# Kernel optimization log

Measured on AMD Instinct MI355X. Metric: run time of the kernel, lower is better.

## Reference

```python
import jax, jax.numpy as jnp
import numpy as np

N = 30000; E = 480000; B = 32
IN_H = 129; IN_P = 15; HID = 64; HEADS = 8; OUT = 129


def gat_conv(x, src, dst, edge_attr, W, a_src, a_dst, We, a_e, bias, concat):
    # PyG GATConv with edge_dim, add_self_loops=True (fill_value='mean'), negative_slope=0.2
    n = x.shape[0]
    H, C = a_src.shape
    ones = jnp.ones((src.shape[0],), x.dtype)
    deg = jax.ops.segment_sum(ones, dst, num_segments=n)
    ea_mean = jax.ops.segment_sum(edge_attr, dst, num_segments=n) / jnp.clip(deg, 1.0)[:, None]
    loop = jnp.arange(n, dtype=src.dtype)
    s = jnp.concatenate([src, loop])
    t = jnp.concatenate([dst, loop])
    ea = jnp.concatenate([edge_attr, ea_mean], axis=0)
    xw = (x @ W).reshape(n, H, C)              # [N,H,C]
    a_s = jnp.sum(xw * a_src, axis=-1)         # [N,H]
    a_d = jnp.sum(xw * a_dst, axis=-1)         # [N,H]
    ew = (ea @ We).reshape(-1, H, C)           # [E2,H,C]
    a_ed = jnp.sum(ew * a_e, axis=-1)          # [E2,H]
    alpha = jax.nn.leaky_relu(a_s[s] + a_d[t] + a_ed, 0.2)
    amax = jax.ops.segment_max(alpha, t, num_segments=n)   # every node has a self-loop
    expa = jnp.exp(alpha - amax[t])
    denom = jax.ops.segment_sum(expa, t, num_segments=n)
    alpha = expa / denom[t]                    # segment softmax over dst
    out = jax.ops.segment_sum(xw[s] * alpha[..., None], t, num_segments=n)  # [N,H,C]
    out = out.reshape(n, H * C) if concat else jnp.mean(out, axis=1)
    return out + bias


def setup_inputs():
    key = jax.random.key(0)
    ks = jax.random.split(key, 40)
    g = lambda k, s: (jax.random.normal(k, s, jnp.float32) * (1.0 / np.sqrt(s[0])))
    d = {}
    d['x_hrtf'] = jax.random.normal(ks[0], (N, IN_H), jnp.float32)
    d['x_pos'] = jax.random.normal(ks[1], (N, IN_P), jnp.float32)
    d['edge_attr_hrtf'] = jax.random.normal(ks[2], (E, 1), jnp.float32)
    d['edge_attr_pos'] = jax.random.normal(ks[3], (E, 1), jnp.float32)
    # hrtf branch, layer 1 (heads=8, concat)
    d['W1h'] = g(ks[4], (IN_H, HEADS * HID)); d['as1h'] = g(ks[5], (HEADS, HID)); d['ad1h'] = g(ks[6], (HEADS, HID))
    d['We1h'] = g(ks[7], (1, HEADS * HID)); d['ae1h'] = g(ks[8], (HEADS, HID)); d['b1h'] = jnp.zeros((HEADS * HID,), jnp.float32)
    # hrtf branch, layer 2 (heads=1, mean)
    d['W2h'] = g(ks[9], (HEADS * HID, OUT)); d['as2h'] = g(ks[10], (1, OUT)); d['ad2h'] = g(ks[11], (1, OUT))
    d['We2h'] = g(ks[12], (1, OUT)); d['ae2h'] = g(ks[13], (1, OUT)); d['b2h'] = jnp.zeros((OUT,), jnp.float32)
    # pos branch, layer 1
    d['W1p'] = g(ks[14], (IN_P, HEADS * HID)); d['as1p'] = g(ks[15], (HEADS, HID)); d['ad1p'] = g(ks[16], (HEADS, HID))
    d['We1p'] = g(ks[17], (1, HEADS * HID)); d['ae1p'] = g(ks[18], (HEADS, HID)); d['b1p'] = jnp.zeros((HEADS * HID,), jnp.float32)
    # pos branch, layer 2
    d['W2p'] = g(ks[19], (HEADS * HID, OUT)); d['as2p'] = g(ks[20], (1, OUT)); d['ad2p'] = g(ks[21], (1, OUT))
    d['We2p'] = g(ks[22], (1, OUT)); d['ae2p'] = g(ks[23], (1, OUT)); d['b2p'] = jnp.zeros((OUT,), jnp.float32)
    # final fc
    d['Wfc'] = g(ks[24], (2 * OUT, 129)); d['bfc'] = jnp.zeros((129,), jnp.float32)
    d['edge_index_hrtf'] = jax.random.randint(ks[25], (2, E), 0, N, jnp.int32)
    d['edge_index_pos'] = jax.random.randint(ks[26], (2, E), 0, N, jnp.int32)
    d['batch'] = ((jnp.arange(N) * B) // N).astype(jnp.int32)  # sorted, equal-sized graphs
    d['num_graphs'] = B
    return d


def reference(x_hrtf, x_pos, edge_attr_hrtf, edge_attr_pos, W1h, as1h, ad1h, We1h, ae1h, b1h, W2h, as2h, ad2h, We2h, ae2h, b2h, W1p, as1p, ad1p, We1p, ae1p, b1p, W2p, as2p, ad2p, We2p, ae2p, b2p, Wfc, bfc, edge_index_hrtf, edge_index_pos, batch, num_graphs):
    sh, th = edge_index_hrtf[0], edge_index_hrtf[1]
    sp, tp = edge_index_pos[0], edge_index_pos[1]
    h = jax.nn.elu(gat_conv(x_hrtf, sh, th, edge_attr_hrtf, W1h, as1h, ad1h, We1h, ae1h, b1h, True))
    h = gat_conv(h, sh, th, edge_attr_hrtf, W2h, as2h, ad2h, We2h, ae2h, b2h, False)
    p = jax.nn.elu(gat_conv(x_pos, sp, tp, edge_attr_pos, W1p, as1p, ad1p, We1p, ae1p, b1p, True))
    p = gat_conv(p, sp, tp, edge_attr_pos, W2p, as2p, ad2p, We2p, ae2p, b2p, False)
    counts = jax.ops.segment_sum(jnp.ones_like(batch), batch, num_segments=num_graphs)
    last = jnp.cumsum(counts) - 1              # last node index of each graph
    z = jnp.concatenate([h[last], p[last]], axis=-1)
    z = z @ Wfc + bfc
    return z[:, None, :]                       # [B,1,129]
```

## Files before the change

### kernel.cpp

```cpp
#include <hip/hip_runtime.h>

#define N_NODES 30000
#define N_EDGES 480000
#define NB      32
#define HEADS   8
#define F1      512
#define OUT_C   129
#define OUT_S   132
#define W1TS    132

#define CAP1   1024
#define MAXD   64
#define NZREG  (8 + 2 * CAP1 + 2 * NB)

#define SHIFT1 12.0f
#define SHIFT2 20.0f

__device__ __forceinline__ float lrelu(float a) { return a > 0.f ? a : 0.2f * a; }

__device__ __forceinline__ int graph_of(int v) { return (int)(((unsigned)v * 2u) / 1875u); }
__device__ __forceinline__ int last_of(int b) { return (int)((((unsigned)(b + 1) * 1875u) + 1u) / 2u) - 1; }
__device__ __forceinline__ bool is_last_node(int v) { return v == last_of(graph_of(v)); }

__global__ void k_prep(const float* We1h, const float* ae1h,
                       const float* We1p, const float* ae1p,
                       const float* We2h, const float* ae2h,
                       const float* We2p, const float* ae2p,
                       const float* __restrict__ W1h, const float* __restrict__ W1p,
                       const float* as1h, const float* as1p,
                       const float* ad1h, const float* ad1p,
                       float* k12, float* __restrict__ w_as, float* __restrict__ w_ad,
                       int* __restrict__ zreg, int* __restrict__ inv1) {
    int gid = blockIdx.x * 256 + threadIdx.x;
    if (gid < 15000) ((int4*)inv1)[gid] = make_int4(-1, -1, -1, -1);
    if (gid < NZREG) zreg[gid] = 0;
    if (blockIdx.x == 0) {
        int t = threadIdx.x;
        if (t < 8) {
            float s = 0.f;
            for (int c = 0; c < 64; c++) s += We1h[t * 64 + c] * ae1h[t * 64 + c];
            k12[t] = s;
        } else if (t < 16) {
            int h = t - 8;
            float s = 0.f;
            for (int c = 0; c < 64; c++) s += We1p[h * 64 + c] * ae1p[h * 64 + c];
            k12[8 + h] = s;
        } else if (t == 16) {
            float s = 0.f;
            for (int c = 0; c < OUT_C; c++) s += We2h[c] * ae2h[c];
            k12[16] = s;
        } else if (t == 17) {
            float s = 0.f;
            for (int c = 0; c < OUT_C; c++) s += We2p[c] * ae2p[c];
            k12[17] = s;
        }
    }
    if (blockIdx.x >= 64 && blockIdx.x < 96) {
        int bb = blockIdx.x - 64;
        int br = bb >> 4, type = (bb >> 3) & 1, h = bb & 7;
        const float* W1 = br ? W1p : W1h;
        const float* a  = type ? (br ? ad1p : ad1h) : (br ? as1p : as1h);
        float* outp = (type ? w_ad : w_as) + (size_t)(br * 8 + h) * W1TS;
        int K = br ? 15 : 129;
        int d = threadIdx.x;
        if (d < K) {
            float s = 0.f;
            for (int c = 0; c < 64; c++) s += W1[(size_t)d * F1 + h * 64 + c] * a[h * 64 + c];
            outp[d] = s;
        }
    }
}

__global__ __launch_bounds__(256) void k_scan2(const int* __restrict__ ei_h,
        const int* __restrict__ ei_p, const float* __restrict__ ea_h,
        const float* __restrict__ ea_p, int* inv1,
        int* degcnt2, int* eb2v, float* eb2e) {
    int br = blockIdx.y;
    const int* ei = br ? ei_p : ei_h;
    const float* ea = br ? ea_p : ea_h;
    const int* src = ei; const int* dst = ei + N_EDGES;
    inv1 += br * N_NODES;
    degcnt2 += br * NB; eb2v += br * NB * MAXD; eb2e += br * NB * MAXD;
    int tid = threadIdx.x;
    if (blockIdx.x == 0 && tid < NB) inv1[last_of(tid)] = -2;
    int base = (blockIdx.x * 256 + tid) * 4;
    if (base >= N_EDGES) return;
    int4 d = *(const int4*)(dst + base);
    int dv[4] = {d.x, d.y, d.z, d.w};
#pragma unroll
    for (int q = 0; q < 4; q++) {
        if (is_last_node(dv[q])) {
            int e = base + q;
            int b = graph_of(dv[q]);
            int slot = atomicAdd(degcnt2 + b, 1);
            if (slot < MAXD) { eb2v[b * MAXD + slot] = src[e]; eb2e[b * MAXD + slot] = ea[e]; }
            inv1[src[e]] = -2;
        }
    }
}

__global__ __launch_bounds__(256) void k_compact1(int* inv1, int* nodes1, int* cnt) {
    __shared__ int s_v[256];
    __shared__ int s_n, s_base;
    int br = blockIdx.y;
    inv1 += br * N_NODES; nodes1 += br * CAP1;
    int* cntp = cnt + br * 4 + 0;
    int tid = threadIdx.x;
    if (tid == 0) s_n = 0;
    __syncthreads();
    int base = (blockIdx.x * 256 + tid) * 4;
    if (base < N_NODES) {
        int4 w = *(const int4*)(inv1 + base);
        int vv[4] = {w.x, w.y, w.z, w.w};
#pragma unroll
        for (int q = 0; q < 4; q++) {
            if (vv[q] == -2) {
                int p = atomicAdd(&s_n, 1);
                if (p < 256) s_v[p] = base + q;
            }
        }
    }
    __syncthreads();
    int n = s_n; if (n > 256) n = 256;
    if (tid == 0) s_base = atomicAdd(cntp, n);
    __syncthreads();
    for (int q = tid; q < n; q += 256) {
        int j = s_base + q;
        if (j < CAP1) { inv1[s_v[q]] = j; nodes1[j] = s_v[q]; }
    }
}

__global__ __launch_bounds__(256) void k_scan1(const int* __restrict__ ei_h,
        const int* __restrict__ ei_p, const float* __restrict__ ea_h,
        const float* __restrict__ ea_p, const int* __restrict__ inv1,
        int* degcnt1, int* ebv1, float* ebe1) {
    int br = blockIdx.y;
    const int* ei = br ? ei_p : ei_h;
    const float* ea = br ? ea_p : ea_h;
    const int* src = ei; const int* dst = ei + N_EDGES;
    inv1 += br * N_NODES;
    degcnt1 += br * CAP1; ebv1 += (size_t)br * CAP1 * MAXD; ebe1 += (size_t)br * CAP1 * MAXD;
    int tid = threadIdx.x;
    int base = (blockIdx.x * 256 + tid) * 4;
    if (base >= N_EDGES) return;
    int4 d = *(const int4*)(dst + base);
    int dv[4] = {d.x, d.y, d.z, d.w};
#pragma unroll
    for (int q = 0; q < 4; q++) {
        int jj = inv1[dv[q]];
        if (jj >= 0) {
            int e = base + q;
            int slot = atomicAdd(degcnt1 + jj, 1);
            if (slot < MAXD) { ebv1[jj * MAXD + slot] = src[e]; ebe1[jj * MAXD + slot] = ea[e]; }
        }
    }
}

__global__ __launch_bounds__(256) void k_agg1x(const int* __restrict__ ebv1,
        const float* __restrict__ ebe1, const int* __restrict__ degcnt1,
        const int* __restrict__ nodes1, const int* cnt,
        const float* __restrict__ x_h, const float* __restrict__ x_p,
        const float* __restrict__ w_as, const float* __restrict__ w_ad,
        const float* __restrict__ k12, const float* __restrict__ b1h,
        const float* __restrict__ b1p, const float* __restrict__ W1h,
        const float* __restrict__ W1p, const float* __restrict__ W2h,
        const float* __restrict__ W2p, const float* __restrict__ as2h,
        const float* __restrict__ as2p, const float* __restrict__ ad2h,
        const float* __restrict__ ad2p,
        float* __restrict__ xw2, float* __restrict__ as2v, float* __restrict__ ad2all) {
    __shared__ float s_x[MAXD + 9][W1TS];
    __shared__ int   s_v[MAXD + 1];
    __shared__ float s_e[MAXD + 1];
    __shared__ float s_ex[(MAXD + 1) * 8];
    __shared__ float s_den[8];
    __shared__ float s_adh[8];
    __shared__ float s_k1[8];
    __shared__ float s_h1[F1];
    __shared__ float s_row[OUT_S];
    int br = blockIdx.y;
    const float* x    = br ? x_p : x_h;
    const float* b1   = br ? b1p : b1h;
    const float* W1   = br ? W1p : W1h;
    const float* W2   = br ? W2p : W2h;
    const float* as2w = br ? as2p : as2h;
    const float* ad2w = br ? ad2p : ad2h;
    const float* wasb = w_as + (size_t)br * 8 * W1TS;
    const float* wadb = w_ad + (size_t)br * 8 * W1TS;
    int K = br ? 15 : 129;
    int n1 = cnt[br * 4 + 0]; if (n1 > CAP1) n1 = CAP1;
    int j = blockIdx.x;
    if (j >= n1) return;
    int tid = threadIdx.x;
    int deg = degcnt1[br * CAP1 + j]; if (deg > MAXD) deg = MAXD;
    const int*   ebv = ebv1 + ((size_t)br * CAP1 + j) * MAXD;
    const float* ebe = ebe1 + ((size_t)br * CAP1 + j) * MAXD;
    if (tid < deg) { s_v[tid] = ebv[tid]; s_e[tid] = ebe[tid]; }
    if (tid == 0) s_v[deg] = nodes1[br * CAP1 + j];
    if (tid >= 72 && tid < 80) s_k1[tid - 72] = k12[br * 8 + (tid - 72)];
    __syncthreads();
    int total = deg + 1;
    for (int k = tid >> 6; k < total; k += 4) {
        const float* xr = x + (size_t)s_v[k] * K;
        for (int d = (tid & 63); d < K; d += 64) s_x[k][d] = xr[d];
    }
    __syncthreads();
    if (tid < 64) {
        float part = (tid < deg) ? s_e[tid] : 0.f;
#pragma unroll
        for (int o = 32; o > 0; o >>= 1) part += __shfl_down(part, o);
        if (tid == 0) s_e[deg] = part / fmaxf((float)deg, 1.f);
    }
    for (int t = tid; t < total * 8 + 8; t += 256) {
        int k, h; const float* wv;
        if (t < total * 8) { k = t >> 3; h = t & 7; wv = wasb + (size_t)h * W1TS; }
        else               { k = deg; h = t - total * 8; wv = wadb + (size_t)h * W1TS; }
        float dot = 0.f;
        for (int d = 0; d < K; d++) dot += s_x[k][d] * wv[d];
        if (t < total * 8) s_ex[t] = dot; else s_adh[h] = dot;
    }
    __syncthreads();
    for (int t = tid; t < total * 8; t += 256) {
        int k = t >> 3, h = t & 7;
        float a = lrelu(s_ex[t] + s_adh[h] + s_e[k] * s_k1[h]);
        s_ex[t] = __expf(a - SHIFT1);
    }
    __syncthreads();
    if (tid >= 192 && tid < 200) {
        int h = tid - 192;
        float d = 0.f;
        for (int k = 0; k < total; k++) d += s_ex[k * 8 + h];
        s_den[h] = d;
    }
    if (tid < K) {
        float acc[8];
#pragma unroll
        for (int h = 0; h < 8; h++) acc[h] = 0.f;
        for (int k = 0; k < total; k++) {
            float xv = s_x[k][tid];
#pragma unroll
            for (int h = 0; h < 8; h++) acc[h] += s_ex[k * 8 + h] * xv;
        }
#pragma unroll
        for (int h = 0; h < 8; h++) s_x[MAXD + 1 + h][tid] = acc[h];
    }
    __syncthreads();
    {
        int h0 = tid >> 6, h1i = h0 + 4;
        float a0 = 0.f, a1 = 0.f;
        for (int d = 0; d < K; d++) {
            float xa0 = s_x[MAXD + 1 + h0][d];
            float xa1 = s_x[MAXD + 1 + h1i][d];
            a0 += xa0 * W1[(size_t)d * F1 + tid];
            a1 += xa1 * W1[(size_t)d * F1 + tid + 256];
        }
        float v0 = a0 / s_den[h0] + b1[tid];
        float v1 = a1 / s_den[h1i] + b1[tid + 256];
        s_h1[tid]       = v0 > 0.f ? v0 : (__expf(v0) - 1.f);
        s_h1[tid + 256] = v1 > 0.f ? v1 : (__expf(v1) - 1.f);
    }
    __syncthreads();
    if (tid < OUT_C) {
        float a = 0.f;
        for (int k = 0; k < F1; k++) a += s_h1[k] * W2[(size_t)k * OUT_C + tid];
        s_row[tid] = a;
        xw2[((size_t)br * CAP1 + j) * OUT_S + tid] = a;
    }
    __syncthreads();
    if (tid < 128) {
        int w = tid >> 6, l = tid & 63;
        const float* av = w ? ad2w : as2w;
        float p = s_row[l] * av[l] + s_row[64 + l] * av[64 + l];
        if (l == 0) p += s_row[128] * av[128];
#pragma unroll
        for (int o = 32; o > 0; o >>= 1) p += __shfl_down(p, o);
        if (l == 0) {
            if (w) ad2all[br * CAP1 + j] = p;
            else   as2v[br * CAP1 + j] = p;
        }
    }
}

__global__ __launch_bounds__(256) void k_agg2fc(const int* __restrict__ eb2v,
        const float* __restrict__ eb2e, const int* __restrict__ degcnt2,
        const int* __restrict__ inv1, const int* cnt,
        const float* __restrict__ as2v, const float* __restrict__ ad2all,
        const float* __restrict__ k12, const float* __restrict__ b2h,
        const float* __restrict__ b2p, const float* __restrict__ xw2,
        const float* __restrict__ Wfc, const float* __restrict__ bfc,
        float* __restrict__ out) {
    __shared__ int   s_j[MAXD + 1];
    __shared__ float s_e[MAXD + 1];
    __shared__ float s_ex[MAXD + 1];
    __shared__ float s_den;
    __shared__ float hcat[2 * OUT_C];
    int b = blockIdx.x;
    int tid = threadIdx.x;
    for (int br = 0; br < 2; br++) {
        const float* b2 = br ? b2p : b2h;
        const int* inv1b = inv1 + br * N_NODES;
        const float* as2vb = as2v + br * CAP1;
        const float* ad2b = ad2all + br * CAP1;
        const float* xw2b = xw2 + (size_t)br * CAP1 * OUT_S;
        float k2 = k12[16 + br];
        int deg = degcnt2[br * NB + b]; if (deg > MAXD) deg = MAXD;
        if (tid < deg) {
            s_j[tid] = inv1b[eb2v[(br * NB + b) * MAXD + tid]];
            s_e[tid] = eb2e[(br * NB + b) * MAXD + tid];
        }
        if (tid == 0) s_j[deg] = inv1b[last_of(b)];
        __syncthreads();
        if (tid < 64) {
            float part = (tid < deg) ? s_e[tid] : 0.f;
#pragma unroll
            for (int o = 32; o > 0; o >>= 1) part += __shfl_down(part, o);
            if (tid == 0) s_e[deg] = part / fmaxf((float)deg, 1.f);
        }
        __syncthreads();
        int total = deg + 1;
        float adv = ad2b[s_j[deg]];
        for (int k = tid; k < total; k += 256)
            s_ex[k] = __expf(lrelu(as2vb[s_j[k]] + adv + s_e[k] * k2) - SHIFT2);
        __syncthreads();
        if (tid == 0) {
            float d = 0.f;
            for (int k = 0; k < total; k++) d += s_ex[k];
            s_den = d;
        }
        __syncthreads();
        if (tid < OUT_C) {
            float acc = 0.f;
            for (int k = 0; k < total; k++)
                acc += s_ex[k] * xw2b[(size_t)s_j[k] * OUT_S + tid];
            hcat[br * OUT_C + tid] = acc / s_den + b2[tid];
        }
        __syncthreads();
    }
    if (tid < OUT_C) {
        float s = bfc[tid];
        for (int k = 0; k < 2 * OUT_C; k++) s += hcat[k] * Wfc[k * OUT_C + tid];
        out[b * OUT_C + tid] = s;
    }
}

extern "C" void kernel_launch(void* const* d_in, const int* in_sizes, int n_in,
                              void* d_out, int out_size, void* d_ws, size_t ws_size,
                              hipStream_t stream) {
    const float* x_h  = (const float*)d_in[0];
    const float* x_p  = (const float*)d_in[1];
    const float* ea_h = (const float*)d_in[2];
    const float* ea_p = (const float*)d_in[3];
    const float* W1h  = (const float*)d_in[4];
    const float* as1h = (const float*)d_in[5];
    const float* ad1h = (const float*)d_in[6];
    const float* We1h = (const float*)d_in[7];
    const float* ae1h = (const float*)d_in[8];
    const float* b1h  = (const float*)d_in[9];
    const float* W2h  = (const float*)d_in[10];
    const float* as2h = (const float*)d_in[11];
    const float* ad2h = (const float*)d_in[12];
    const float* We2h = (const float*)d_in[13];
    const float* ae2h = (const float*)d_in[14];
    const float* b2h  = (const float*)d_in[15];
    const float* W1p  = (const float*)d_in[16];
    const float* as1p = (const float*)d_in[17];
    const float* ad1p = (const float*)d_in[18];
    const float* We1p = (const float*)d_in[19];
    const float* ae1p = (const float*)d_in[20];
    const float* b1p  = (const float*)d_in[21];
    const float* W2p  = (const float*)d_in[22];
    const float* as2p = (const float*)d_in[23];
    const float* ad2p = (const float*)d_in[24];
    const float* We2p = (const float*)d_in[25];
    const float* ae2p = (const float*)d_in[26];
    const float* b2p  = (const float*)d_in[27];
    const float* Wfc  = (const float*)d_in[28];
    const float* bfc  = (const float*)d_in[29];
    const int*   ei_h = (const int*)d_in[30];
    const int*   ei_p = (const int*)d_in[31];

    char* wsb = (char*)d_ws;
    size_t off = 0;
    auto alloc = [&](size_t elems) -> char* {
        char* p = wsb + off;
        off += ((elems * 4 + 255) / 256) * 256;
        return p;
    };
    float*    k12     = (float*)alloc(18);
    int*      zreg    = (int*)alloc(NZREG);
    int*      cnt     = zreg;
    int*      degcnt1 = zreg + 8;
    int*      degcnt2 = zreg + 8 + 2 * CAP1;
    int*      inv1    = (int*)alloc(2 * N_NODES);
    int*      nodes1  = (int*)alloc(2 * CAP1);
    int*      ebv1    = (int*)alloc(2 * (size_t)CAP1 * MAXD);
    float*    ebe1    = (float*)alloc(2 * (size_t)CAP1 * MAXD);
    int*      eb2v    = (int*)alloc(2 * NB * MAXD);
    float*    eb2e    = (float*)alloc(2 * NB * MAXD);
    float*    w_as    = (float*)alloc(2 * 8 * W1TS);
    float*    w_ad    = (float*)alloc(2 * 8 * W1TS);
    float*    xw2     = (float*)alloc(2 * (size_t)CAP1 * OUT_S);
    float*    as2v    = (float*)alloc(2 * CAP1);
    float*    ad2all  = (float*)alloc(2 * CAP1);
    if (off > ws_size) return;

    const int EBLK4 = (N_EDGES / 4 + 255) / 256;
    const int NBLK4 = (N_NODES / 4 + 255) / 256;

    k_prep<<<96, 256, 0, stream>>>(
        We1h, ae1h, We1p, ae1p, We2h, ae2h, We2p, ae2p,
        W1h, W1p, as1h, as1p, ad1h, ad1p,
        k12, w_as, w_ad, zreg, inv1);
    k_scan2<<<dim3(EBLK4, 2), 256, 0, stream>>>(ei_h, ei_p, ea_h, ea_p, inv1,
                                                degcnt2, eb2v, eb2e);
    k_compact1<<<dim3(NBLK4, 2), 256, 0, stream>>>(inv1, nodes1, cnt);
    k_scan1<<<dim3(EBLK4, 2), 256, 0, stream>>>(ei_h, ei_p, ea_h, ea_p, inv1,
                                                degcnt1, ebv1, ebe1);
    k_agg1x<<<dim3(CAP1, 2), 256, 0, stream>>>(ebv1, ebe1, degcnt1, nodes1, cnt,
                                               x_h, x_p, w_as, w_ad, k12, b1h, b1p,
                                               W1h, W1p, W2h, W2p, as2h, as2p, ad2h, ad2p,
                                               xw2, as2v, ad2all);
    k_agg2fc<<<NB, 256, 0, stream>>>(eb2v, eb2e, degcnt2, inv1, cnt,
                                     as2v, ad2all, k12, b2h, b2p, xw2, Wfc, bfc, (float*)d_out);
}
```

Before: 90.51 us.

## Split fused per-node aggregation into batched GEMM kernels with weight reuse

The monolithic per-node kernel that aggregated neighbours and then multiplied each node's features by W1 and W2 is split into three kernels: aggregation only, a tiled layer-1 GEMM over 32-node tiles per head, and a layer-2 GEMM processing two nodes per block against a transposed W2 prepared in the prep kernel. The goal is to reuse weight loads across many nodes instead of re-reading W1/W2 from global memory per node. In exchange it adds two kernel launches and writes and reads intermediate buffers (normalized aggregates, h1) through global memory.

```diff
diff --git a/kernel.cpp b/kernel.cpp
--- a/kernel.cpp
+++ b/kernel.cpp
@@ -12,6 +12,7 @@
 #define CAP1   1024
 #define MAXD   64
 #define NZREG  (8 + 2 * CAP1 + 2 * NB)
+#define TJ     32
 
 #define SHIFT1 12.0f
 #define SHIFT2 20.0f
@@ -27,13 +28,20 @@
                        const float* We2h, const float* ae2h,
                        const float* We2p, const float* ae2p,
                        const float* __restrict__ W1h, const float* __restrict__ W1p,
+                       const float* __restrict__ W2h, const float* __restrict__ W2p,
                        const float* as1h, const float* as1p,
                        const float* ad1h, const float* ad1p,
                        float* k12, float* __restrict__ w_as, float* __restrict__ w_ad,
-                       int* __restrict__ zreg, int* __restrict__ inv1) {
+                       float* __restrict__ W2t2, int* __restrict__ zreg,
+                       int* __restrict__ inv1) {
     int gid = blockIdx.x * 256 + threadIdx.x;
     if (gid < 15000) ((int4*)inv1)[gid] = make_int4(-1, -1, -1, -1);
     if (gid < NZREG) zreg[gid] = 0;
+    if (gid < 512 * OUT_C) {
+        int k = gid / OUT_C, c = gid % OUT_C;
+        W2t2[c * 512 + k] = W2h[gid];
+        W2t2[512 * OUT_C + c * 512 + k] = W2p[gid];
+    }
     if (blockIdx.x == 0) {
         int t = threadIdx.x;
         if (t < 8) {
@@ -55,8 +63,8 @@
             k12[17] = s;
         }
     }
-    if (blockIdx.x >= 64 && blockIdx.x < 96) {
-        int bb = blockIdx.x - 64;
+    if (blockIdx.x >= 128 && blockIdx.x < 160) {
+        int bb = blockIdx.x - 128;
         int br = bb >> 4, type = (bb >> 3) & 1, h = bb & 7;
         const float* W1 = br ? W1p : W1h;
         const float* a  = type ? (br ? ad1p : ad1h) : (br ? as1p : as1h);
@@ -156,34 +164,21 @@
     }
 }
 
-__global__ __launch_bounds__(256) void k_agg1x(const int* __restrict__ ebv1,
+__global__ __launch_bounds__(256) void k_agg1(const int* __restrict__ ebv1,
         const float* __restrict__ ebe1, const int* __restrict__ degcnt1,
         const int* __restrict__ nodes1, const int* cnt,
         const float* __restrict__ x_h, const float* __restrict__ x_p,
         const float* __restrict__ w_as, const float* __restrict__ w_ad,
-        const float* __restrict__ k12, const float* __restrict__ b1h,
-        const float* __restrict__ b1p, const float* __restrict__ W1h,
-        const float* __restrict__ W1p, const float* __restrict__ W2h,
-        const float* __restrict__ W2p, const float* __restrict__ as2h,
-        const float* __restrict__ as2p, const float* __restrict__ ad2h,
-        const float* __restrict__ ad2p,
-        float* __restrict__ xw2, float* __restrict__ as2v, float* __restrict__ ad2all) {
-    __shared__ float s_x[MAXD + 9][W1TS];
+        const float* __restrict__ k12, float* __restrict__ xaggn) {
+    __shared__ float s_x[MAXD + 1][W1TS];
     __shared__ int   s_v[MAXD + 1];
     __shared__ float s_e[MAXD + 1];
     __shared__ float s_ex[(MAXD + 1) * 8];
     __shared__ float s_den[8];
     __shared__ float s_adh[8];
     __shared__ float s_k1[8];
-    __shared__ float s_h1[F1];
-    __shared__ float s_row[OUT_S];
     int br = blockIdx.y;
     const float* x    = br ? x_p : x_h;
-    const float* b1   = br ? b1p : b1h;
-    const float* W1   = br ? W1p : W1h;
-    const float* W2   = br ? W2p : W2h;
-    const float* as2w = br ? as2p : as2h;
-    const float* ad2w = br ? ad2p : ad2h;
     const float* wasb = w_as + (size_t)br * 8 * W1TS;
     const float* wadb = w_ad + (size_t)br * 8 * W1TS;
     int K = br ? 15 : 129;
@@ -213,7 +208,7 @@
     for (int t = tid; t < total * 8 + 8; t += 256) {
         int k, h; const float* wv;
         if (t < total * 8) { k = t >> 3; h = t & 7; wv = wasb + (size_t)h * W1TS; }
-        else               { k = deg; h = t - total * 8; wv = wadb + (size_t)h * W1TS; }
+        else               { k = total - 1; h = t - total * 8; wv = wadb + (size_t)h * W1TS; }
         float dot = 0.f;
         for (int d = 0; d < K; d++) dot += s_x[k][d] * wv[d];
         if (t < total * 8) s_ex[t] = dot; else s_adh[h] = dot;
@@ -225,12 +220,12 @@
         s_ex[t] = __expf(a - SHIFT1);
     }
     __syncthreads();
-    if (tid >= 192 && tid < 200) {
-        int h = tid - 192;
+    if (tid < 8) {
         float d = 0.f;
-        for (int k = 0; k < total; k++) d += s_ex[k * 8 + h];
-        s_den[h] = d;
-    }
+        for (int k = 0; k < total; k++) d += s_ex[k * 8 + tid];
+        s_den[tid] = 1.f / d;
+    }
+    __syncthreads();
     if (tid < K) {
         float acc[8];
 #pragma unroll
@@ -241,41 +236,130 @@
             for (int h = 0; h < 8; h++) acc[h] += s_ex[k * 8 + h] * xv;
         }
 #pragma unroll
-        for (int h = 0; h < 8; h++) s_x[MAXD + 1 + h][tid] = acc[h];
-    }
-    __syncthreads();
-    {
-        int h0 = tid >> 6, h1i = h0 + 4;
-        float a0 = 0.f, a1 = 0.f;
-        for (int d = 0; d < K; d++) {
-            float xa0 = s_x[MAXD + 1 + h0][d];
-            float xa1 = s_x[MAXD + 1 + h1i][d];
-            a0 += xa0 * W1[(size_t)d * F1 + tid];
-            a1 += xa1 * W1[(size_t)d * F1 + tid + 256];
-        }
-        float v0 = a0 / s_den[h0] + b1[tid];
-        float v1 = a1 / s_den[h1i] + b1[tid + 256];
-        s_h1[tid]       = v0 > 0.f ? v0 : (__expf(v0) - 1.f);
-        s_h1[tid + 256] = v1 > 0.f ? v1 : (__expf(v1) - 1.f);
-    }
-    __syncthreads();
-    if (tid < OUT_C) {
-        float a = 0.f;
-        for (int k = 0; k < F1; k++) a += s_h1[k] * W2[(size_t)k * OUT_C + tid];
-        s_row[tid] = a;
-        xw2[((size_t)br * CAP1 + j) * OUT_S + tid] = a;
-    }
-    __syncthreads();
-    if (tid < 128) {
-        int w = tid >> 6, l = tid & 63;
-        const float* av = w ? ad2w : as2w;
-        float p = s_row[l] * av[l] + s_row[64 + l] * av[64 + l];
-        if (l == 0) p += s_row[128] * av[128];
-#pragma unroll
-        for (int o = 32; o > 0; o >>= 1) p += __shfl_down(p, o);
-        if (l == 0) {
-            if (w) ad2all[br * CAP1 + j] = p;
-            else   as2v[br * CAP1 + j] = p;
+        for (int h = 0; h < 8; h++)
+            xaggn[((size_t)(br * 8 + h) * CAP1 + j) * W1TS + tid] = acc[h] * s_den[h];
+    }
+}
+
+__global__ __launch_bounds__(256) void k_h1gemm(const float* __restrict__ xaggn,
+        const int* cnt, const float* __restrict__ W1h, const float* __restrict__ W1p,
+        const float* __restrict__ b1h, const float* __restrict__ b1p,
+        float* __restrict__ h1) {
+    __shared__ float s_a[TJ][W1TS];
+    __shared__ float s_b[OUT_C][64];
+    int br = blockIdx.y;
+    const float* W1 = br ? W1p : W1h;
+    const float* b1 = br ? b1p : b1h;
+    int K = br ? 15 : 129;
+    int n1 = cnt[br * 4 + 0]; if (n1 > CAP1) n1 = CAP1;
+    int jt = blockIdx.x >> 3, h = blockIdx.x & 7;
+    int j0 = jt * TJ;
+    if (j0 >= n1) return;
+    int tid = threadIdx.x;
+    const float4* ap = (const float4*)(xaggn + ((size_t)(br * 8 + h) * CAP1 + j0) * W1TS);
+    for (int t = tid; t < TJ * W1TS / 4; t += 256) ((float4*)&s_a[0][0])[t] = ap[t];
+    for (int t = tid; t < K * 64; t += 256) {
+        int d = t >> 6, c = t & 63;
+        s_b[d][c] = W1[(size_t)d * F1 + h * 64 + c];
+    }
+    __syncthreads();
+    int r0 = (tid >> 6) * 8, c = tid & 63;
+    float acc[8];
+#pragma unroll
+    for (int rr = 0; rr < 8; rr++) acc[rr] = 0.f;
+    for (int d = 0; d < K; d++) {
+        float bv = s_b[d][c];
+#pragma unroll
+        for (int rr = 0; rr < 8; rr++) acc[rr] += s_a[r0 + rr][d] * bv;
+    }
+    float bb = b1[h * 64 + c];
+#pragma unroll
+    for (int rr = 0; rr < 8; rr++) {
+        int j = j0 + r0 + rr;
+        if (j < n1) {
+            float v = acc[rr] + bb;
+            h1[((size_t)br * CAP1 + j) * F1 + h * 64 + c] = v > 0.f ? v : (__expf(v) - 1.f);
+        }
+    }
+}
+
+__global__ __launch_bounds__(256) void k_gemm2a(const float* __restrict__ h1,
+        const float* __restrict__ W2t2, const float* __restrict__ as2h,
+        const float* __restrict__ as2p, const float* __restrict__ ad2h,
+        const float* __restrict__ ad2p, const int* cnt,
+        float* __restrict__ xw2, float* __restrict__ as2v, float* __restrict__ ad2all) {
+    __shared__ float hs[2][512];
+    __shared__ float part[4][2][132];
+    __shared__ float rows_[2][132];
+    __shared__ float redS[4], redD[4];
+    int br = blockIdx.y;
+    const float* W2t = W2t2 + (size_t)br * 512 * OUT_C;
+    const float* as2w = br ? as2p : as2h;
+    const float* ad2w = br ? ad2p : ad2h;
+    h1 += (size_t)br * CAP1 * F1;
+    xw2 += (size_t)br * CAP1 * OUT_S;
+    as2v += br * CAP1; ad2all += br * CAP1;
+    int n1 = cnt[br * 4 + 0]; if (n1 > CAP1) n1 = CAP1;
+    int j0 = blockIdx.x * 2;
+    if (j0 >= n1) return;
+    int tid = threadIdx.x;
+    for (int r = 0; r < 2; r++) {
+        int j = j0 + r;
+        for (int k = tid; k < 512; k += 256)
+            hs[r][k] = (j < n1) ? h1[(size_t)j * F1 + k] : 0.f;
+    }
+    __syncthreads();
+    int w = tid >> 6, l = tid & 63;
+    float a0[2] = {0.f, 0.f}, a1[2] = {0.f, 0.f}, a2[2] = {0.f, 0.f};
+    const float* w0p = W2t + (size_t)l * 512;
+    const float* w1p = W2t + (size_t)(64 + l) * 512;
+    const float* w2p = W2t + (size_t)128 * 512;
+    int kbase = w * 128;
+#pragma unroll 4
+    for (int kk = 0; kk < 128; kk += 4) {
+        int k = kbase + kk;
+        float4 wv0 = *(const float4*)(w0p + k);
+        float4 wv1 = *(const float4*)(w1p + k);
+        float4 wv2 = *(const float4*)(w2p + k);
+#pragma unroll
+        for (int r = 0; r < 2; r++) {
+            float4 hv = *(const float4*)&hs[r][k];
+            a0[r] += hv.x * wv0.x + hv.y * wv0.y + hv.z * wv0.z + hv.w * wv0.w;
+            a1[r] += hv.x * wv1.x + hv.y * wv1.y + hv.z * wv1.z + hv.w * wv1.w;
+            a2[r] += hv.x * wv2.x + hv.y * wv2.y + hv.z * wv2.z + hv.w * wv2.w;
+        }
+    }
+#pragma unroll
+    for (int r = 0; r < 2; r++) {
+        part[w][r][l] = a0[r];
+        part[w][r][64 + l] = a1[r];
+        if (l == 0) part[w][r][128] = a2[r];
+    }
+    __syncthreads();
+    for (int idx = tid; idx < 2 * OUT_C; idx += 256) {
+        int r = idx >= OUT_C;
+        int c = idx - r * OUT_C;
+        float s = part[0][r][c] + part[1][r][c] + part[2][r][c] + part[3][r][c];
+        rows_[r][c] = s;
+        int j = j0 + r;
+        if (j < n1) xw2[(size_t)j * OUT_S + c] = s;
+    }
+    __syncthreads();
+    int r = w >> 1;
+    int c = tid & 127;
+    float rv = rows_[r][c];
+    float ps = rv * as2w[c];
+    float pd = rv * ad2w[c];
+    if (c == 0) { ps += rows_[r][128] * as2w[128]; pd += rows_[r][128] * ad2w[128]; }
+#pragma unroll
+    for (int o = 32; o > 0; o >>= 1) { ps += __shfl_down(ps, o); pd += __shfl_down(pd, o); }
+    if (l == 0) { redS[w] = ps; redD[w] = pd; }
+    __syncthreads();
+    if (tid < 2) {
+        int j = j0 + tid;
+        if (j < n1) {
+            as2v[j] = redS[2 * tid] + redS[2 * tid + 1];
+            ad2all[j] = redD[2 * tid] + redD[2 * tid + 1];
         }
     }
 }
@@ -398,6 +482,9 @@
     float*    eb2e    = (float*)alloc(2 * NB * MAXD);
     float*    w_as    = (float*)alloc(2 * 8 * W1TS);
     float*    w_ad    = (float*)alloc(2 * 8 * W1TS);
+    float*    xaggn   = (float*)alloc(2 * 8 * (size_t)CAP1 * W1TS);
+    float*    h1      = (float*)alloc(2 * (size_t)CAP1 * F1);
+    float*    W2t2    = (float*)alloc(2 * 512 * OUT_C);
     float*    xw2     = (float*)alloc(2 * (size_t)CAP1 * OUT_S);
     float*    as2v    = (float*)alloc(2 * CAP1);
     float*    ad2all  = (float*)alloc(2 * CAP1);
@@ -406,19 +493,21 @@
     const int EBLK4 = (N_EDGES / 4 + 255) / 256;
     const int NBLK4 = (N_NODES / 4 + 255) / 256;
 
-    k_prep<<<96, 256, 0, stream>>>(
+    k_prep<<<259, 256, 0, stream>>>(
         We1h, ae1h, We1p, ae1p, We2h, ae2h, We2p, ae2p,
-        W1h, W1p, as1h, as1p, ad1h, ad1p,
-        k12, w_as, w_ad, zreg, inv1);
+        W1h, W1p, W2h, W2p, as1h, as1p, ad1h, ad1p,
+        k12, w_as, w_ad, W2t2, zreg, inv1);
     k_scan2<<<dim3(EBLK4, 2), 256, 0, stream>>>(ei_h, ei_p, ea_h, ea_p, inv1,
                                                 degcnt2, eb2v, eb2e);
     k_compact1<<<dim3(NBLK4, 2), 256, 0, stream>>>(inv1, nodes1, cnt);
     k_scan1<<<dim3(EBLK4, 2), 256, 0, stream>>>(ei_h, ei_p, ea_h, ea_p, inv1,
                                                 degcnt1, ebv1, ebe1);
-    k_agg1x<<<dim3(CAP1, 2), 256, 0, stream>>>(ebv1, ebe1, degcnt1, nodes1, cnt,
-                                               x_h, x_p, w_as, w_ad, k12, b1h, b1p,
-                                               W1h, W1p, W2h, W2p, as2h, as2p, ad2h, ad2p,
-                                               xw2, as2v, ad2all);
+    k_agg1<<<dim3(CAP1, 2), 256, 0, stream>>>(ebv1, ebe1, degcnt1, nodes1, cnt,
+                                              x_h, x_p, w_as, w_ad, k12, xaggn);
+    k_h1gemm<<<dim3((CAP1 / TJ) * 8, 2), 256, 0, stream>>>(xaggn, cnt, W1h, W1p,
+                                                           b1h, b1p, h1);
+    k_gemm2a<<<dim3(CAP1 / 2, 2), 256, 0, stream>>>(h1, W2t2, as2h, as2p, ad2h, ad2p,
+                                                    cnt, xw2, as2v, ad2all);
     k_agg2fc<<<NB, 256, 0, stream>>>(eb2v, eb2e, degcnt2, inv1, cnt,
                                      as2v, ad2all, k12, b2h, b2p, xw2, Wfc, bfc, (float*)d_out);
 }
```

Measured after the change: 110.2 us. +21.8%, slower.

## Fuse node compaction into edge scan and batch four layer-1 nodes per block

Applied to the files above, without the earlier changes.

The separate compaction kernel is removed. The edge scan now claims the source nodes it needs with atomicCAS and assigns their compact indices in the same pass, which saves one launch and one pass over the node array. The layer-1 aggregation kernel now processes four nodes per block, one per wavefront. Each W1 and W2 row loaded from global memory is reused across the four nodes, which cuts weight traffic by four, and neighbor features are read directly from global memory instead of being staged in shared memory. The costs are a lower block count, more per-thread accumulator registers, and the assumption that inv1 is initialised to -1 before the claim.

```diff
diff --git a/kernel.cpp b/kernel.cpp
--- a/kernel.cpp
+++ b/kernel.cpp
@@ -12,6 +12,7 @@
 #define CAP1   1024
 #define MAXD   64
 #define NZREG  (8 + 2 * CAP1 + 2 * NB)
+#define JB     4
 
 #define SHIFT1 12.0f
 #define SHIFT2 20.0f
@@ -73,60 +74,59 @@
 
 __global__ __launch_bounds__(256) void k_scan2(const int* __restrict__ ei_h,
         const int* __restrict__ ei_p, const float* __restrict__ ea_h,
-        const float* __restrict__ ea_p, int* inv1,
+        const float* __restrict__ ea_p, int* inv1, int* nodes1, int* cnt,
         int* degcnt2, int* eb2v, float* eb2e) {
+    __shared__ int s_claim[128];
+    __shared__ int s_n, s_base;
     int br = blockIdx.y;
     const int* ei = br ? ei_p : ei_h;
     const float* ea = br ? ea_p : ea_h;
     const int* src = ei; const int* dst = ei + N_EDGES;
-    inv1 += br * N_NODES;
-    degcnt2 += br * NB; eb2v += br * NB * MAXD; eb2e += br * NB * MAXD;
-    int tid = threadIdx.x;
-    if (blockIdx.x == 0 && tid < NB) inv1[last_of(tid)] = -2;
-    int base = (blockIdx.x * 256 + tid) * 4;
-    if (base >= N_EDGES) return;
-    int4 d = *(const int4*)(dst + base);
-    int dv[4] = {d.x, d.y, d.z, d.w};
-#pragma unroll
-    for (int q = 0; q < 4; q++) {
-        if (is_last_node(dv[q])) {
-            int e = base + q;
-            int b = graph_of(dv[q]);
-            int slot = atomicAdd(degcnt2 + b, 1);
-            if (slot < MAXD) { eb2v[b * MAXD + slot] = src[e]; eb2e[b * MAXD + slot] = ea[e]; }
-            inv1[src[e]] = -2;
-        }
-    }
-}
-
-__global__ __launch_bounds__(256) void k_compact1(int* inv1, int* nodes1, int* cnt) {
-    __shared__ int s_v[256];
-    __shared__ int s_n, s_base;
-    int br = blockIdx.y;
-    inv1 += br * N_NODES; nodes1 += br * CAP1;
-    int* cntp = cnt + br * 4 + 0;
+    int* inv1b = inv1 + br * N_NODES;
+    int* nodes1b = nodes1 + br * CAP1;
+    int* cntp = cnt + br * 4;
+    int* dc2 = degcnt2 + br * NB;
+    int* e2v = eb2v + br * NB * MAXD;
+    float* e2e = eb2e + br * NB * MAXD;
     int tid = threadIdx.x;
     if (tid == 0) s_n = 0;
     __syncthreads();
+    auto claim = [&](int v) {
+        if (atomicCAS(&inv1b[v], -1, -3) == -1) {
+            int p = atomicAdd(&s_n, 1);
+            if (p < 128) s_claim[p] = v;
+            else {
+                int j = atomicAdd(cntp, 1);
+                if (j < CAP1) { nodes1b[j] = v; inv1b[v] = j; }
+                else inv1b[v] = -1;
+            }
+        }
+    };
+    if (blockIdx.x == 0 && tid < NB) claim(last_of(tid));
     int base = (blockIdx.x * 256 + tid) * 4;
-    if (base < N_NODES) {
-        int4 w = *(const int4*)(inv1 + base);
-        int vv[4] = {w.x, w.y, w.z, w.w};
+    if (base < N_EDGES) {
+        int4 d4 = *(const int4*)(dst + base);
+        int dv[4] = {d4.x, d4.y, d4.z, d4.w};
 #pragma unroll
         for (int q = 0; q < 4; q++) {
-            if (vv[q] == -2) {
-                int p = atomicAdd(&s_n, 1);
-                if (p < 256) s_v[p] = base + q;
-            }
-        }
-    }
-    __syncthreads();
-    int n = s_n; if (n > 256) n = 256;
+            if (is_last_node(dv[q])) {
+                int e = base + q;
+                int b = graph_of(dv[q]);
+                int slot = atomicAdd(dc2 + b, 1);
+                if (slot < MAXD) { e2v[b * MAXD + slot] = src[e]; e2e[b * MAXD + slot] = ea[e]; }
+                claim(src[e]);
+            }
+        }
+    }
+    __syncthreads();
+    int n = s_n; if (n > 128) n = 128;
     if (tid == 0) s_base = atomicAdd(cntp, n);
     __syncthreads();
     for (int q = tid; q < n; q += 256) {
         int j = s_base + q;
-        if (j < CAP1) { inv1[s_v[q]] = j; nodes1[j] = s_v[q]; }
+        int v = s_claim[q];
+        if (j < CAP1) { nodes1b[j] = v; inv1b[v] = j; }
+        else inv1b[v] = -1;
     }
 }
 
@@ -138,7 +138,7 @@
     const int* ei = br ? ei_p : ei_h;
     const float* ea = br ? ea_p : ea_h;
     const int* src = ei; const int* dst = ei + N_EDGES;
-    inv1 += br * N_NODES;
+    const int* inv1b = inv1 + br * N_NODES;
     degcnt1 += br * CAP1; ebv1 += (size_t)br * CAP1 * MAXD; ebe1 += (size_t)br * CAP1 * MAXD;
     int tid = threadIdx.x;
     int base = (blockIdx.x * 256 + tid) * 4;
@@ -147,8 +147,8 @@
     int dv[4] = {d.x, d.y, d.z, d.w};
 #pragma unroll
     for (int q = 0; q < 4; q++) {
-        int jj = inv1[dv[q]];
-        if (jj >= 0) {
+        int jj = inv1b[dv[q]];
+        if (jj >= 0 && jj < CAP1) {
             int e = base + q;
             int slot = atomicAdd(degcnt1 + jj, 1);
             if (slot < MAXD) { ebv1[jj * MAXD + slot] = src[e]; ebe1[jj * MAXD + slot] = ea[e]; }
@@ -156,127 +156,209 @@
     }
 }
 
-__global__ __launch_bounds__(256) void k_agg1x(const int* __restrict__ ebv1,
+__global__ __launch_bounds__(256) void k_fuse1(const int* __restrict__ ebv1,
         const float* __restrict__ ebe1, const int* __restrict__ degcnt1,
         const int* __restrict__ nodes1, const int* cnt,
         const float* __restrict__ x_h, const float* __restrict__ x_p,
         const float* __restrict__ w_as, const float* __restrict__ w_ad,
-        const float* __restrict__ k12, const float* __restrict__ b1h,
-        const float* __restrict__ b1p, const float* __restrict__ W1h,
-        const float* __restrict__ W1p, const float* __restrict__ W2h,
-        const float* __restrict__ W2p, const float* __restrict__ as2h,
-        const float* __restrict__ as2p, const float* __restrict__ ad2h,
-        const float* __restrict__ ad2p,
+        const float* __restrict__ k12,
+        const float* __restrict__ W1h, const float* __restrict__ W1p,
+        const float* __restrict__ b1h, const float* __restrict__ b1p,
+        const float* __restrict__ W2h, const float* __restrict__ W2p,
+        const float* __restrict__ as2h, const float* __restrict__ as2p,
+        const float* __restrict__ ad2h, const float* __restrict__ ad2p,
         float* __restrict__ xw2, float* __restrict__ as2v, float* __restrict__ ad2all) {
-    __shared__ float s_x[MAXD + 9][W1TS];
-    __shared__ int   s_v[MAXD + 1];
-    __shared__ float s_e[MAXD + 1];
-    __shared__ float s_ex[(MAXD + 1) * 8];
-    __shared__ float s_den[8];
-    __shared__ float s_adh[8];
+    __shared__ float s_was[8][W1TS];
+    __shared__ float s_wad[8][W1TS];
     __shared__ float s_k1[8];
-    __shared__ float s_h1[F1];
-    __shared__ float s_row[OUT_S];
+    __shared__ int   s_v[JB][MAXD + 1];
+    __shared__ float s_e[JB][MAXD + 1];
+    __shared__ float s_as[JB][MAXD + 1][8];
+    __shared__ float s_ad[JB][8];
+    __shared__ float s_invden[JB][8];
+    __shared__ int   s_deg[JB];
+    __shared__ float s_xagg[JB][8][W1TS];
+    __shared__ float s_h1[JB][F1];
+    __shared__ float s_row[JB][W1TS];
     int br = blockIdx.y;
     const float* x    = br ? x_p : x_h;
+    const float* W1   = br ? W1p : W1h;
     const float* b1   = br ? b1p : b1h;
-    const float* W1   = br ? W1p : W1h;
     const float* W2   = br ? W2p : W2h;
     const float* as2w = br ? as2p : as2h;
     const float* ad2w = br ? ad2p : ad2h;
-    const float* wasb = w_as + (size_t)br * 8 * W1TS;
-    const float* wadb = w_ad + (size_t)br * 8 * W1TS;
     int K = br ? 15 : 129;
-    int n1 = cnt[br * 4 + 0]; if (n1 > CAP1) n1 = CAP1;
-    int j = blockIdx.x;
-    if (j >= n1) return;
+    int n1 = cnt[br * 4]; if (n1 > CAP1) n1 = CAP1;
+    int j0 = blockIdx.x * JB;
+    if (j0 >= n1) return;
     int tid = threadIdx.x;
-    int deg = degcnt1[br * CAP1 + j]; if (deg > MAXD) deg = MAXD;
-    const int*   ebv = ebv1 + ((size_t)br * CAP1 + j) * MAXD;
-    const float* ebe = ebe1 + ((size_t)br * CAP1 + j) * MAXD;
-    if (tid < deg) { s_v[tid] = ebv[tid]; s_e[tid] = ebe[tid]; }
-    if (tid == 0) s_v[deg] = nodes1[br * CAP1 + j];
-    if (tid >= 72 && tid < 80) s_k1[tid - 72] = k12[br * 8 + (tid - 72)];
-    __syncthreads();
-    int total = deg + 1;
-    for (int k = tid >> 6; k < total; k += 4) {
-        const float* xr = x + (size_t)s_v[k] * K;
-        for (int d = (tid & 63); d < K; d += 64) s_x[k][d] = xr[d];
-    }
-    __syncthreads();
-    if (tid < 64) {
-        float part = (tid < deg) ? s_e[tid] : 0.f;
+    for (int t = tid; t < 8 * W1TS; t += 256) {
+        int h = t / W1TS, d = t % W1TS;
+        float vs = 0.f, vd = 0.f;
+        if (d < K) {
+            vs = w_as[(size_t)(br * 8 + h) * W1TS + d];
+            vd = w_ad[(size_t)(br * 8 + h) * W1TS + d];
+        }
+        s_was[h][d] = vs;
+        s_wad[h][d] = vd;
+    }
+    if (tid < 8) s_k1[tid] = k12[br * 8 + tid];
+    if (tid < JB) {
+        int j = j0 + tid;
+        int dg = 0;
+        if (j < n1) { dg = degcnt1[br * CAP1 + j]; if (dg > MAXD) dg = MAXD; }
+        s_deg[tid] = dg;
+    }
+    __syncthreads();
+    for (int t = tid; t < JB * (MAXD + 1); t += 256) {
+        int jj = t / (MAXD + 1), k = t % (MAXD + 1);
+        int j = j0 + jj;
+        if (j < n1) {
+            int dg = s_deg[jj];
+            if (k < dg) {
+                s_v[jj][k] = ebv1[((size_t)(br * CAP1 + j)) * MAXD + k];
+                s_e[jj][k] = ebe1[((size_t)(br * CAP1 + j)) * MAXD + k];
+            } else if (k == dg) {
+                s_v[jj][k] = nodes1[br * CAP1 + j];
+            }
+        }
+    }
+    __syncthreads();
+    int w = tid >> 6, lane = tid & 63;
+    int jA = j0 + w;
+    if (jA < n1) {
+        int dg = s_deg[w];
+        float part = (lane < dg) ? s_e[w][lane] : 0.f;
 #pragma unroll
         for (int o = 32; o > 0; o >>= 1) part += __shfl_down(part, o);
-        if (tid == 0) s_e[deg] = part / fmaxf((float)deg, 1.f);
-    }
-    for (int t = tid; t < total * 8 + 8; t += 256) {
-        int k, h; const float* wv;
-        if (t < total * 8) { k = t >> 3; h = t & 7; wv = wasb + (size_t)h * W1TS; }
-        else               { k = deg; h = t - total * 8; wv = wadb + (size_t)h * W1TS; }
-        float dot = 0.f;
-        for (int d = 0; d < K; d++) dot += s_x[k][d] * wv[d];
-        if (t < total * 8) s_ex[t] = dot; else s_adh[h] = dot;
-    }
-    __syncthreads();
-    for (int t = tid; t < total * 8; t += 256) {
-        int k = t >> 3, h = t & 7;
-        float a = lrelu(s_ex[t] + s_adh[h] + s_e[k] * s_k1[h]);
-        s_ex[t] = __expf(a - SHIFT1);
-    }
-    __syncthreads();
-    if (tid >= 192 && tid < 200) {
-        int h = tid - 192;
-        float d = 0.f;
-        for (int k = 0; k < total; k++) d += s_ex[k * 8 + h];
-        s_den[h] = d;
-    }
-    if (tid < K) {
-        float acc[8];
-#pragma unroll
-        for (int h = 0; h < 8; h++) acc[h] = 0.f;
-        for (int k = 0; k < total; k++) {
-            float xv = s_x[k][tid];
-#pragma unroll
-            for (int h = 0; h < 8; h++) acc[h] += s_ex[k * 8 + h] * xv;
-        }
-#pragma unroll
-        for (int h = 0; h < 8; h++) s_x[MAXD + 1 + h][tid] = acc[h];
+        if (lane == 0) s_e[w][dg] = part / fmaxf((float)dg, 1.f);
+        for (int k = 0; k <= dg; k++) {
+            int v = s_v[w][k];
+            float xd0 = (lane < K) ? x[(size_t)v * K + lane] : 0.f;
+            float xd1 = (64 + lane < K) ? x[(size_t)v * K + 64 + lane] : 0.f;
+            float xd2 = (lane == 0 && K > 128) ? x[(size_t)v * K + 128] : 0.f;
+            float pa[8];
+#pragma unroll
+            for (int h = 0; h < 8; h++)
+                pa[h] = xd0 * s_was[h][lane] + xd1 * s_was[h][64 + lane] + xd2 * s_was[h][128];
+#pragma unroll
+            for (int h = 0; h < 8; h++) {
+                float p = pa[h];
+#pragma unroll
+                for (int o = 32; o > 0; o >>= 1) p += __shfl_down(p, o);
+                if (lane == 0) s_as[w][k][h] = p;
+            }
+            if (k == dg) {
+#pragma unroll
+                for (int h = 0; h < 8; h++)
+                    pa[h] = xd0 * s_wad[h][lane] + xd1 * s_wad[h][64 + lane] + xd2 * s_wad[h][128];
+#pragma unroll
+                for (int h = 0; h < 8; h++) {
+                    float p = pa[h];
+#pragma unroll
+                    for (int o = 32; o > 0; o >>= 1) p += __shfl_down(p, o);
+                    if (lane == 0) s_ad[w][h] = p;
+                }
+            }
+        }
+    }
+    __syncthreads();
+    for (int t = tid; t < JB * (MAXD + 1) * 8; t += 256) {
+        int jj = t / ((MAXD + 1) * 8), r = t % ((MAXD + 1) * 8);
+        int k = r >> 3, h = r & 7;
+        if (j0 + jj < n1 && k <= s_deg[jj]) {
+            float a = lrelu(s_as[jj][k][h] + s_ad[jj][h] + s_e[jj][k] * s_k1[h]);
+            s_as[jj][k][h] = __expf(a - SHIFT1);
+        }
+    }
+    __syncthreads();
+    if (tid < JB * 8) {
+        int jj = tid >> 3, h = tid & 7;
+        if (j0 + jj < n1) {
+            float d = 0.f;
+            int tot = s_deg[jj] + 1;
+            for (int k = 0; k < tot; k++) d += s_as[jj][k][h];
+            s_invden[jj][h] = 1.f / d;
+        }
+    }
+    __syncthreads();
+    if (jA < n1) {
+        int dg = s_deg[w];
+        float acc0[8], acc1[8], acc2[8];
+#pragma unroll
+        for (int h = 0; h < 8; h++) { acc0[h] = 0.f; acc1[h] = 0.f; acc2[h] = 0.f; }
+        for (int k = 0; k <= dg; k++) {
+            int v = s_v[w][k];
+            float xd0 = (lane < K) ? x[(size_t)v * K + lane] : 0.f;
+            float xd1 = (64 + lane < K) ? x[(size_t)v * K + 64 + lane] : 0.f;
+            float xd2 = (lane == 0 && K > 128) ? x[(size_t)v * K + 128] : 0.f;
+#pragma unroll
+            for (int h = 0; h < 8; h++) {
+                float ex = s_as[w][k][h];
+                acc0[h] += ex * xd0; acc1[h] += ex * xd1; acc2[h] += ex * xd2;
+            }
+        }
+#pragma unroll
+        for (int h = 0; h < 8; h++) {
+            if (lane < K) s_xagg[w][h][lane] = acc0[h];
+            if (64 + lane < K) s_xagg[w][h][64 + lane] = acc1[h];
+            if (lane == 0 && K > 128) s_xagg[w][h][128] = acc2[h];
+        }
     }
     __syncthreads();
     {
-        int h0 = tid >> 6, h1i = h0 + 4;
-        float a0 = 0.f, a1 = 0.f;
+        int c0 = tid, c1 = tid + 256;
+        int h0 = c0 >> 6, h1i = c1 >> 6;
+        float a0[JB], a1[JB];
+#pragma unroll
+        for (int jj = 0; jj < JB; jj++) { a0[jj] = 0.f; a1[jj] = 0.f; }
         for (int d = 0; d < K; d++) {
-            float xa0 = s_x[MAXD + 1 + h0][d];
-            float xa1 = s_x[MAXD + 1 + h1i][d];
-            a0 += xa0 * W1[(size_t)d * F1 + tid];
-            a1 += xa1 * W1[(size_t)d * F1 + tid + 256];
-        }
-        float v0 = a0 / s_den[h0] + b1[tid];
-        float v1 = a1 / s_den[h1i] + b1[tid + 256];
-        s_h1[tid]       = v0 > 0.f ? v0 : (__expf(v0) - 1.f);
-        s_h1[tid + 256] = v1 > 0.f ? v1 : (__expf(v1) - 1.f);
+            float w0 = W1[(size_t)d * F1 + c0];
+            float w1 = W1[(size_t)d * F1 + c1];
+#pragma unroll
+            for (int jj = 0; jj < JB; jj++) {
+                a0[jj] += s_xagg[jj][h0][d] * w0;
+                a1[jj] += s_xagg[jj][h1i][d] * w1;
+            }
+        }
+        float bb0 = b1[c0], bb1 = b1[c1];
+#pragma unroll
+        for (int jj = 0; jj < JB; jj++) {
+            if (j0 + jj < n1) {
+                float v0 = a0[jj] * s_invden[jj][h0] + bb0;
+                float v1 = a1[jj] * s_invden[jj][h1i] + bb1;
+                s_h1[jj][c0] = v0 > 0.f ? v0 : (__expf(v0) - 1.f);
+                s_h1[jj][c1] = v1 > 0.f ? v1 : (__expf(v1) - 1.f);
+            }
+        }
     }
     __syncthreads();
     if (tid < OUT_C) {
-        float a = 0.f;
-        for (int k = 0; k < F1; k++) a += s_h1[k] * W2[(size_t)k * OUT_C + tid];
-        s_row[tid] = a;
-        xw2[((size_t)br * CAP1 + j) * OUT_S + tid] = a;
-    }
-    __syncthreads();
-    if (tid < 128) {
-        int w = tid >> 6, l = tid & 63;
-        const float* av = w ? ad2w : as2w;
-        float p = s_row[l] * av[l] + s_row[64 + l] * av[64 + l];
-        if (l == 0) p += s_row[128] * av[128];
-#pragma unroll
-        for (int o = 32; o > 0; o >>= 1) p += __shfl_down(p, o);
-        if (l == 0) {
-            if (w) ad2all[br * CAP1 + j] = p;
-            else   as2v[br * CAP1 + j] = p;
-        }
+        float a[JB];
+#pragma unroll
+        for (int jj = 0; jj < JB; jj++) a[jj] = 0.f;
+        for (int k = 0; k < F1; k++) {
+            float w2 = W2[(size_t)k * OUT_C + tid];
+#pragma unroll
+            for (int jj = 0; jj < JB; jj++) a[jj] += s_h1[jj][k] * w2;
+        }
+#pragma unroll
+        for (int jj = 0; jj < JB; jj++) {
+            int j = j0 + jj;
+            if (j < n1) {
+                s_row[jj][tid] = a[jj];
+                xw2[((size_t)br * CAP1 + j) * OUT_S + tid] = a[jj];
+            }
+        }
+    }
+    __syncthreads();
+    if (jA < n1) {
+        float ps = s_row[w][lane] * as2w[lane] + s_row[w][64 + lane] * as2w[64 + lane];
+        float pd = s_row[w][lane] * ad2w[lane] + s_row[w][64 + lane] * ad2w[64 + lane];
+        if (lane == 0) { ps += s_row[w][128] * as2w[128]; pd += s_row[w][128] * ad2w[128]; }
+#pragma unroll
+        for (int o = 32; o > 0; o >>= 1) { ps += __shfl_down(ps, o); pd += __shfl_down(pd, o); }
+        if (lane == 0) { as2v[br * CAP1 + jA] = ps; ad2all[br * CAP1 + jA] = pd; }
     }
 }
 
@@ -404,21 +486,20 @@
     if (off > ws_size) return;
 
     const int EBLK4 = (N_EDGES / 4 + 255) / 256;
-    const int NBLK4 = (N_NODES / 4 + 255) / 256;
 
     k_prep<<<96, 256, 0, stream>>>(
         We1h, ae1h, We1p, ae1p, We2h, ae2h, We2p, ae2p,
         W1h, W1p, as1h, as1p, ad1h, ad1p,
         k12, w_as, w_ad, zreg, inv1);
     k_scan2<<<dim3(EBLK4, 2), 256, 0, stream>>>(ei_h, ei_p, ea_h, ea_p, inv1,
-                                                degcnt2, eb2v, eb2e);
-    k_compact1<<<dim3(NBLK4, 2), 256, 0, stream>>>(inv1, nodes1, cnt);
+                                                nodes1, cnt, degcnt2, eb2v, eb2e);
     k_scan1<<<dim3(EBLK4, 2), 256, 0, stream>>>(ei_h, ei_p, ea_h, ea_p, inv1,
                                                 degcnt1, ebv1, ebe1);
-    k_agg1x<<<dim3(CAP1, 2), 256, 0, stream>>>(ebv1, ebe1, degcnt1, nodes1, cnt,
-                                               x_h, x_p, w_as, w_ad, k12, b1h, b1p,
-                                               W1h, W1p, W2h, W2p, as2h, as2p, ad2h, ad2p,
-                                               xw2, as2v, ad2all);
+    k_fuse1<<<dim3(CAP1 / JB, 2), 256, 0, stream>>>(ebv1, ebe1, degcnt1, nodes1, cnt,
+                                                    x_h, x_p, w_as, w_ad, k12,
+                                                    W1h, W1p, b1h, b1p, W2h, W2p,
+                                                    as2h, as2p, ad2h, ad2p,
+                                                    xw2, as2v, ad2all);
     k_agg2fc<<<NB, 256, 0, stream>>>(eb2v, eb2e, degcnt2, inv1, cnt,
                                      as2v, ad2all, k12, b2h, b2p, xw2, Wfc, bfc, (float*)d_out);
 }
```

New measurement: 150.3 us. 66.1% more time.
